# Performance work log

Hardware: AMD Instinct MI355X
Metric: run time of the kernel (lower is better)

The kernel has to match this reference:

```python
import jax, jax.numpy as jnp
import numpy as np


def _perceive(x):
    """Depthwise 3x3 perception: per channel emit (identity, dx, dy), matching
    tf.nn.depthwise_conv2d with kernel repeated along the in-channel axis, so
    output channel ordering is [c0_I, c0_dx, c0_dy, c1_I, ...]."""
    C = x.shape[-1]
    _i = jnp.array([0.0, 1.0, 0.0], dtype=x.dtype)
    I = jnp.outer(_i, _i)
    dx = jnp.outer(jnp.array([1.0, 2.0, 1.0], dtype=x.dtype),
                   jnp.array([-1.0, 0.0, 1.0], dtype=x.dtype)) / 8.0
    dy = dx.T
    base = jnp.stack([I, dx, dy], axis=-1)[:, :, None, :]  # [3,3,1,3]
    kernel = jnp.tile(base, (1, 1, 1, C))                   # [3,3,1,3C]
    # grouped conv with feature_group_count=C == depthwise conv, multiplier 3
    y = jax.lax.conv_general_dilated(
        x, kernel, window_strides=(1, 1), padding='SAME',
        dimension_numbers=('NHWC', 'HWIO', 'NHWC'), feature_group_count=C)
    return y  # [B,H,W,3C]


def setup_inputs() -> dict:
    key = jax.random.key(0)
    ks = jax.random.split(key, 6)
    B, H, W, C = 16, 256, 256, 16
    x = jax.random.normal(ks[0], (B, H, W, C), dtype=jnp.float32)
    # update mask: tf.random.normal(...) <= fire_rate (0.5), per pixel
    update_mask = jax.random.normal(ks[1], (B, H, W, 1), dtype=jnp.float32) <= 0.5
    # 1x1 conv weights (glorot-ish scale). NOTE: the original zero-initializes
    # w3/b3; we use small random values so the op is numerically non-trivial.
    w1 = jax.random.normal(ks[2], (3 * C, 4 * C), dtype=jnp.float32) / np.sqrt(3 * C)
    b1 = jnp.zeros((4 * C,), dtype=jnp.float32)
    w2 = jax.random.normal(ks[3], (4 * C, 2 * C), dtype=jnp.float32) / np.sqrt(4 * C)
    b2 = jnp.zeros((2 * C,), dtype=jnp.float32)
    w3 = jax.random.normal(ks[4], (2 * C, C), dtype=jnp.float32) / np.sqrt(2 * C)
    b3 = jnp.zeros((C,), dtype=jnp.float32)
    return {"x": x, "w1": w1, "b1": b1, "w2": w2, "b2": b2,
            "w3": w3, "b3": b3, "update_mask": update_mask}


def reference(x, w1, b1, w2, b2, w3, b3, update_mask):
    step_size = 1.0
    y = _perceive(x)  # [B,H,W,3C]
    h = jnp.tanh(jnp.einsum('bhwc,cd->bhwd', y, w1) + b1)
    h = jnp.tanh(jnp.einsum('bhwc,cd->bhwd', h, w2) + b2)
    dx = (jnp.einsum('bhwc,cd->bhwd', h, w3) + b3) * step_size
    return x + dx * update_mask.astype(x.dtype)
```

## Files before the change

### kernel.cpp

```cpp
#include <hip/hip_runtime.h>
#include <hip/hip_bf16.h>

typedef unsigned int u32;
typedef unsigned short u16;
typedef unsigned char u8;

typedef float f32x16 __attribute__((ext_vector_type(16)));
typedef short bf16x8 __attribute__((ext_vector_type(8)));

#define OFF_A1  0
#define OFF_A1B 18432
#define OFF_WT2 20480
#define OFF_WT3 25600
#define OFF_B3  27648
#define PREP_N  13840

__global__ void probe_kernel(const u16* __restrict__ w1h,
                             const u32* __restrict__ maskw,
                             u32* __restrict__ flags) {
  __shared__ int sg, su8, sbf;
  if (threadIdx.x == 0) { sg = 0; su8 = 0; sbf = 0; }
  __syncthreads();
  int g = 0;
#pragma unroll
  for (int i = 0; i < 8; ++i) {
    u16 h = w1h[threadIdx.x * 8 + i];
    int e = (h >> 7) & 0xFF;
    if (e >= 0xC0) g++;
  }
  if (g) atomicAdd(&sg, g);
  u32 w = maskw[threadIdx.x];
  bool bytes01 = ((w & 0xFEFEFEFEu) == 0u);
  int bsum = (int)(w & 1u) + (int)((w >> 8) & 1u) +
             (int)((w >> 16) & 1u) + (int)((w >> 24) & 1u);
  if (bytes01 && bsum >= 2) atomicAdd(&su8, 1);
  if (w == 0x3F803F80u || w == 0x00003F80u) atomicAdd(&sbf, 1);
  __syncthreads();
  if (threadIdx.x == 0) {
    flags[0] = (sg == 0) ? 1u : 0u;
    flags[1] = (su8 > 0) ? 1u : ((sbf > 0) ? 2u : 4u);
  }
}

__device__ __forceinline__ float bf2f(u16 h) {
  return __uint_as_float(((u32)h) << 16);
}
__device__ __forceinline__ u16 f2bf(float f) {
  u32 u = __float_as_uint(f);
  return (u16)((u + 0x7FFFu + ((u >> 16) & 1u)) >> 16);
}
__device__ __forceinline__ u32 pkbf(float a, float b) {
  u32 ua = __float_as_uint(a) + 0x8000u;
  u32 ub = __float_as_uint(b) + 0x8000u;
  return __builtin_amdgcn_perm(ub, ua, 0x07060302);
}
__device__ __forceinline__ float rdv(const void* s, int i, bool bf) {
  return bf ? bf2f(((const u16*)s)[i]) : ((const float*)s)[i];
}

__global__ void prep_weights(const void* __restrict__ w1, const void* __restrict__ b1,
                             const void* __restrict__ w2, const void* __restrict__ b2,
                             const void* __restrict__ w3, const void* __restrict__ b3,
                             const u32* __restrict__ flags, u8* __restrict__ Wb) {
  int i = blockIdx.x * 256 + threadIdx.x;
  if (i >= PREP_N) return;
  const bool bf = flags[0] != 0;
  if (i < 9216) {
    int off = i >> 10, rem = i & 1023;
    int mt = rem >> 9, hi = (rem >> 8) & 1, l = (rem >> 3) & 31, k8 = i & 7;
    int ch = mt * 32 + l, k = hi * 8 + k8;
    int oi = off / 3, oj = off % 3;
    const float axv[3] = {1.f, 2.f, 1.f};
    const float bxv[3] = {-1.f, 0.f, 1.f};
    float ci  = (oi == 1 && oj == 1) ? 1.f : 0.f;
    float dxv = axv[oi] * bxv[oj] * 0.125f;
    float dyv = axv[oj] * bxv[oi] * 0.125f;
    float v = ci  * rdv(w1, (3 * k + 0) * 64 + ch, bf)
            + dxv * rdv(w1, (3 * k + 1) * 64 + ch, bf)
            + dyv * rdv(w1, (3 * k + 2) * 64 + ch, bf);
    ((u16*)(Wb + OFF_A1))[i] = f2bf(v);
  } else if (i < 10240) {
    int j = i - 9216;
    int mt = j >> 9, l = (j >> 3) & 31;
    ((u16*)(Wb + OFF_A1B))[j] = f2bf(rdv(b1, mt * 32 + l, bf) * 0.0625f);
  } else if (i < 12800) {
    int j = i - 10240, n = j / 80, k = j - n * 80;
    float v;
    if (k < 64) {
      int s = k >> 4, hh = (k >> 3) & 1, q = (k & 7) >> 1, e = k & 1;
      int c = 32 * (s >> 1) + 8 * (2 * (s & 1) + (q >> 1)) + 4 * hh + 2 * (q & 1) + e;
      v = rdv(w2, c * 32 + n, bf);
    } else {
      v = (k == 64) ? rdv(b2, n, bf) : 0.0f;
    }
    ((u16*)(Wb + OFF_WT2))[j] = f2bf(v);
  } else if (i < 13824) {
    int j = i - 12800, n = j >> 5, k = j & 31;
    float v = 0.0f;
    if (n < 16) {
      int cout = (n & 3) + 4 * ((n >> 3) & 1) + 8 * ((n >> 2) & 1);
      int s = k >> 4, hh = (k >> 3) & 1, q = (k & 7) >> 1, e = k & 1;
      int cin = 8 * (2 * s + (q >> 1)) + 4 * hh + 2 * (q & 1) + e;
      v = rdv(w3, cin * 16 + cout, bf);
    }
    ((u16*)(Wb + OFF_WT3))[j] = f2bf(v);
  } else {
    int j = i - 13824;
    ((float*)(Wb + OFF_B3))[j] = rdv(b3, j, bf);
  }
}

__device__ __forceinline__ float fast_tanh(float x) {
  float e = __expf(2.0f * x);
  float r = __builtin_amdgcn_rcpf(e + 1.0f);
  return fmaf(-2.0f, r, 1.0f);
}

union U4 { uint4 q; u32 u[4]; bf16x8 h; float4 f; };

__device__ __forceinline__ void wave_lds_fence() {
  __builtin_amdgcn_wave_barrier();
  __asm__ __volatile__("s_waitcnt lgkmcnt(0)" ::: "memory");
  __builtin_amdgcn_wave_barrier();
}

#define MFMA(a, b, c) __builtin_amdgcn_mfma_f32_32x32x16_bf16((a), (b), (c), 0, 0, 0)

#define XS_STRIDE 8256
#define SCR_OFF   33024
#define SCR_WAVE  5120
#define LDS_TOTAL 53504

template <bool BF16>
__device__ __forceinline__ void nca_body(const void* __restrict__ xv,
                                         const u8* __restrict__ Wb,
                                         const void* __restrict__ maskv, int mw,
                                         void* __restrict__ outv,
                                         u8* __restrict__ xs) {
  const int tid = threadIdx.x;
  const int l   = tid & 63;
  const int wid = tid >> 6;
  const int l31 = l & 31;
  const int hi  = l >> 5;
  const int img   = blockIdx.x >> 7;
  const int r0    = (blockIdx.x & 127) << 1;

  if (tid < 8) {
    int rr = tid >> 1, side = tid & 1;
    uint4 z = make_uint4(0, 0, 0, 0);
    uint4* d = (uint4*)(xs + rr * XS_STRIDE + (side ? 257 : 0) * 32);
    d[0] = z; d[1] = z;
  }
#pragma unroll
  for (int rr = 0; rr < 4; ++rr) {
    int hr = r0 - 1 + rr;
    bool valid = (hr >= 0) && (hr <= 255);
    if (BF16) {
      const u16* src = (const u16*)xv + ((size_t)(img * 256 + hr) << 12);
#pragma unroll
      for (int s = 0; s < 2; ++s) {
        int c = s * 256 + tid;
        uint4 v = make_uint4(0, 0, 0, 0);
        if (valid) v = *(const uint4*)(src + c * 8);
        *(uint4*)(xs + rr * XS_STRIDE + ((c >> 1) + 1) * 32 + (c & 1) * 16) = v;
      }
    } else {
      const float* src = (const float*)xv + ((size_t)(img * 256 + hr) << 12);
#pragma unroll
      for (int k = 0; k < 4; ++k) {
        int q = k * 256 + tid;
        uint2 w = make_uint2(0, 0);
        if (valid) {
          float4 v = *(const float4*)(src + q * 4);
          w.x = pkbf(v.x, v.y); w.y = pkbf(v.z, v.w);
        }
        *(uint2*)(xs + rr * XS_STRIDE + ((q >> 2) + 1) * 32 + (q & 3) * 8) = w;
      }
    }
  }
  __syncthreads();

  const int sr      = wid >> 1;
  const int colbase = (wid & 1) * 128;
  const int gr      = img * 256 + r0 + sr;
  const int growpix = gr << 8;

  bf16x8 A1b[2];
#pragma unroll
  for (int mt = 0; mt < 2; ++mt) {
    U4 t; t.q = *(const uint4*)(Wb + OFF_A1B + ((mt * 2 + hi) * 32 + l31) * 16);
    A1b[mt] = t.h;
  }
  U4 ones; ones.u[0] = ones.u[1] = ones.u[2] = ones.u[3] = 0x3F803F80u;
  const float* B3f = (const float*)(Wb + OFF_B3);
  float4 b3lo = *(const float4*)(B3f + 8 * hi);
  float4 b3hi4 = *(const float4*)(B3f + 8 * hi + 4);
  u8* scr = xs + SCR_OFF + wid * SCR_WAVE;

#pragma unroll
  for (int tp = 0; tp < 2; ++tp) {
#pragma unroll
    for (int u = 0; u < 2; ++u) {
      const int cb = colbase + (tp * 2 + u) * 32;

      f32x16 c0 = {0,0,0,0,0,0,0,0,0,0,0,0,0,0,0,0};
      f32x16 c1 = {0,0,0,0,0,0,0,0,0,0,0,0,0,0,0,0};
      c0 = MFMA(A1b[0], ones.h, c0);
      c1 = MFMA(A1b[1], ones.h, c1);
#pragma unroll
      for (int off = 0; off < 9; ++off) {
        const int oi = off / 3, oj = off % 3;
        U4 bx; bx.q = *(const uint4*)(xs + (sr + oi) * XS_STRIDE +
                                      (cb + l31 + oj) * 32 + hi * 16);
        U4 a0; a0.q = *(const uint4*)(Wb + OFF_A1 + (((off * 2 + 0) * 2 + hi) * 32 + l31) * 16);
        U4 a1; a1.q = *(const uint4*)(Wb + OFF_A1 + (((off * 2 + 1) * 2 + hi) * 32 + l31) * 16);
        c0 = MFMA(a0.h, bx.h, c0);
        c1 = MFMA(a1.h, bx.h, c1);
      }

      u32 o1[16];
#pragma unroll
      for (int g = 0; g < 4; ++g)
#pragma unroll
        for (int pp = 0; pp < 2; ++pp) {
          o1[g * 2 + pp]     = pkbf(fast_tanh(c0[g * 4 + 2 * pp]), fast_tanh(c0[g * 4 + 2 * pp + 1]));
          o1[8 + g * 2 + pp] = pkbf(fast_tanh(c1[g * 4 + 2 * pp]), fast_tanh(c1[g * 4 + 2 * pp + 1]));
        }

      f32x16 c2 = {0,0,0,0,0,0,0,0,0,0,0,0,0,0,0,0};
#pragma unroll
      for (int s = 0; s < 4; ++s) {
        U4 a2; a2.q = *(const uint4*)(Wb + OFF_WT2 + l31 * 160 + s * 32 + hi * 16);
        U4 bfr; bfr.u[0] = o1[4*s]; bfr.u[1] = o1[4*s+1]; bfr.u[2] = o1[4*s+2]; bfr.u[3] = o1[4*s+3];
        c2 = MFMA(a2.h, bfr.h, c2);
      }
      {
        U4 a2; a2.q = *(const uint4*)(Wb + OFF_WT2 + l31 * 160 + 4 * 32 + hi * 16);
        U4 bb; bb.u[0] = hi ? 0u : 0x00003F80u; bb.u[1] = 0; bb.u[2] = 0; bb.u[3] = 0;
        c2 = MFMA(a2.h, bb.h, c2);
      }
      u32 o2[8];
#pragma unroll
      for (int g = 0; g < 4; ++g)
#pragma unroll
        for (int pp = 0; pp < 2; ++pp)
          o2[g * 2 + pp] = pkbf(fast_tanh(c2[g * 4 + 2 * pp]), fast_tanh(c2[g * 4 + 2 * pp + 1]));

      f32x16 c3 = {0,0,0,0,0,0,0,0,0,0,0,0,0,0,0,0};
#pragma unroll
      for (int s = 0; s < 2; ++s) {
        U4 a3; a3.q = *(const uint4*)(Wb + OFF_WT3 + l31 * 64 + s * 32 + hi * 16);
        U4 bfr; bfr.u[0] = o2[4*s]; bfr.u[1] = o2[4*s+1]; bfr.u[2] = o2[4*s+2]; bfr.u[3] = o2[4*s+3];
        c3 = MFMA(a3.h, bfr.h, c3);
      }

      U4 w0, w1;
      w0.f.x = c3[0] + b3lo.x;  w0.f.y = c3[1] + b3lo.y;
      w0.f.z = c3[2] + b3lo.z;  w0.f.w = c3[3] + b3lo.w;
      w1.f.x = c3[4] + b3hi4.x; w1.f.y = c3[5] + b3hi4.y;
      w1.f.z = c3[6] + b3hi4.z; w1.f.w = c3[7] + b3hi4.w;
      u8* sa = scr + (u * 32 + l31) * 80 + hi * 32;
      *(float4*)(sa) = w0.f;
      *(float4*)(sa + 16) = w1.f;
    }
    wave_lds_fence();

    const int cb2 = colbase + tp * 64;
#pragma unroll
    for (int P = 0; P < 4; ++P) {
      const int px_l = P * 16 + (l >> 2);
      const int qd   = l & 3;
      float4 dx = *(const float4*)(scr + px_l * 80 + qd * 16);
      const int gpx = growpix + cb2 + px_l;
      bool ms;
      if (mw == 1)      ms = ((const u8*)maskv)[gpx] != 0;
      else if (mw == 2) ms = ((const u16*)maskv)[gpx] != 0;
      else              ms = ((const u32*)maskv)[gpx] != 0;
      const float mf = ms ? 1.0f : 0.0f;
      const int e = gpx * 16 + qd * 4;
      if (BF16) {
        uint2 xu = *(const uint2*)((const u16*)xv + e);
        float x0 = bf2f((u16)(xu.x & 0xFFFF)), x1 = bf2f((u16)(xu.x >> 16));
        float x2 = bf2f((u16)(xu.y & 0xFFFF)), x3 = bf2f((u16)(xu.y >> 16));
        float o0 = fmaf(dx.x, mf, x0), o1v = fmaf(dx.y, mf, x1);
        float o2v = fmaf(dx.z, mf, x2), o3v = fmaf(dx.w, mf, x3);
        uint2 w; w.x = pkbf(o0, o1v); w.y = pkbf(o2v, o3v);
        *(uint2*)((u16*)outv + e) = w;
      } else {
        float4 xc = *(const float4*)((const float*)xv + e);
        float4 o;
        o.x = fmaf(dx.x, mf, xc.x); o.y = fmaf(dx.y, mf, xc.y);
        o.z = fmaf(dx.z, mf, xc.z); o.w = fmaf(dx.w, mf, xc.w);
        *(float4*)((float*)outv + e) = o;
      }
    }
    wave_lds_fence();
  }
}

__global__ __launch_bounds__(256, 3) void nca_main(const void* __restrict__ xv,
                                                   const u8* __restrict__ Wb,
                                                   const void* __restrict__ maskv,
                                                   const u32* __restrict__ flags,
                                                   void* __restrict__ outv) {
  __shared__ __align__(16) u8 smem[LDS_TOTAL];
  const bool isbf = flags[0] != 0;
  const int mw = (int)flags[1];
  if (isbf) nca_body<true>(xv, Wb, maskv, mw, outv, smem);
  else      nca_body<false>(xv, Wb, maskv, mw, outv, smem);
}

extern "C" void kernel_launch(void* const* d_in, const int* in_sizes, int n_in,
                              void* d_out, int out_size, void* d_ws, size_t ws_size,
                              hipStream_t stream) {
  u32* flags = (u32*)d_ws;
  u8* Wb = (u8*)d_ws + 64;

  probe_kernel<<<1, 256, 0, stream>>>((const u16*)d_in[1], (const u32*)d_in[7], flags);

  prep_weights<<<(PREP_N + 255) / 256, 256, 0, stream>>>(
      d_in[1], d_in[2], d_in[3], d_in[4], d_in[5], d_in[6], flags, Wb);

  const int pixels = in_sizes[7];
  const int blocks = pixels / 512;
  nca_main<<<blocks, 256, 0, stream>>>(d_in[0], Wb, d_in[7], flags, d_out);
}
```

Measured before the change: 216.6 us.

## Fold probe into kernels, write outputs from MFMA registers, drop LDS scratch

```diff
diff --git a/kernel.cpp b/kernel.cpp
--- a/kernel.cpp
+++ b/kernel.cpp
@@ -15,33 +15,6 @@
 #define OFF_B3  27648
 #define PREP_N  13840
 
-__global__ void probe_kernel(const u16* __restrict__ w1h,
-                             const u32* __restrict__ maskw,
-                             u32* __restrict__ flags) {
-  __shared__ int sg, su8, sbf;
-  if (threadIdx.x == 0) { sg = 0; su8 = 0; sbf = 0; }
-  __syncthreads();
-  int g = 0;
-#pragma unroll
-  for (int i = 0; i < 8; ++i) {
-    u16 h = w1h[threadIdx.x * 8 + i];
-    int e = (h >> 7) & 0xFF;
-    if (e >= 0xC0) g++;
-  }
-  if (g) atomicAdd(&sg, g);
-  u32 w = maskw[threadIdx.x];
-  bool bytes01 = ((w & 0xFEFEFEFEu) == 0u);
-  int bsum = (int)(w & 1u) + (int)((w >> 8) & 1u) +
-             (int)((w >> 16) & 1u) + (int)((w >> 24) & 1u);
-  if (bytes01 && bsum >= 2) atomicAdd(&su8, 1);
-  if (w == 0x3F803F80u || w == 0x00003F80u) atomicAdd(&sbf, 1);
-  __syncthreads();
-  if (threadIdx.x == 0) {
-    flags[0] = (sg == 0) ? 1u : 0u;
-    flags[1] = (su8 > 0) ? 1u : ((sbf > 0) ? 2u : 4u);
-  }
-}
-
 __device__ __forceinline__ float bf2f(u16 h) {
   return __uint_as_float(((u32)h) << 16);
 }
@@ -61,10 +34,26 @@
 __global__ void prep_weights(const void* __restrict__ w1, const void* __restrict__ b1,
                              const void* __restrict__ w2, const void* __restrict__ b2,
                              const void* __restrict__ w3, const void* __restrict__ b3,
-                             const u32* __restrict__ flags, u8* __restrict__ Wb) {
+                             u8* __restrict__ Wb) {
+  __shared__ int sg;
+  if (threadIdx.x == 0) sg = 0;
+  __syncthreads();
+  {
+    const u16* w1h = (const u16*)w1;
+    int g = 0;
+#pragma unroll
+    for (int k = 0; k < 8; ++k) {
+      u16 h = w1h[threadIdx.x * 8 + k];
+      int e = (h >> 7) & 0xFF;
+      if (e >= 0xC0) g++;
+    }
+    if (g) atomicAdd(&sg, g);
+  }
+  __syncthreads();
+  const bool bf = (sg == 0);
+
   int i = blockIdx.x * 256 + threadIdx.x;
   if (i >= PREP_N) return;
-  const bool bf = flags[0] != 0;
   if (i < 9216) {
     int off = i >> 10, rem = i & 1023;
     int mt = rem >> 9, hi = (rem >> 8) & 1, l = (rem >> 3) & 31, k8 = i & 7;
@@ -118,32 +107,24 @@
 
 union U4 { uint4 q; u32 u[4]; bf16x8 h; float4 f; };
 
-__device__ __forceinline__ void wave_lds_fence() {
-  __builtin_amdgcn_wave_barrier();
-  __asm__ __volatile__("s_waitcnt lgkmcnt(0)" ::: "memory");
-  __builtin_amdgcn_wave_barrier();
-}
-
 #define MFMA(a, b, c) __builtin_amdgcn_mfma_f32_32x32x16_bf16((a), (b), (c), 0, 0, 0)
 
 #define XS_STRIDE 8256
-#define SCR_OFF   33024
-#define SCR_WAVE  5120
-#define LDS_TOTAL 53504
+#define LDS_TOTAL 33024
 
 template <bool BF16>
 __device__ __forceinline__ void nca_body(const void* __restrict__ xv,
                                          const u8* __restrict__ Wb,
                                          const void* __restrict__ maskv, int mw,
                                          void* __restrict__ outv,
-                                         u8* __restrict__ xs) {
+                                         u8* __restrict__ xs, int wg) {
   const int tid = threadIdx.x;
   const int l   = tid & 63;
   const int wid = tid >> 6;
   const int l31 = l & 31;
   const int hi  = l >> 5;
-  const int img   = blockIdx.x >> 7;
-  const int r0    = (blockIdx.x & 127) << 1;
+  const int img   = wg >> 7;
+  const int r0    = (wg & 127) << 1;
 
   if (tid < 8) {
     int rr = tid >> 1, side = tid & 1;
@@ -193,15 +174,36 @@
   }
   U4 ones; ones.u[0] = ones.u[1] = ones.u[2] = ones.u[3] = 0x3F803F80u;
   const float* B3f = (const float*)(Wb + OFF_B3);
-  float4 b3lo = *(const float4*)(B3f + 8 * hi);
+  float4 b3lo  = *(const float4*)(B3f + 8 * hi);
   float4 b3hi4 = *(const float4*)(B3f + 8 * hi + 4);
-  u8* scr = xs + SCR_OFF + wid * SCR_WAVE;
 
 #pragma unroll
   for (int tp = 0; tp < 2; ++tp) {
 #pragma unroll
     for (int u = 0; u < 2; ++u) {
       const int cb = colbase + (tp * 2 + u) * 32;
+      const int gpx = growpix + cb + l31;
+      const int e = gpx * 16 + hi * 8;
+
+      bool ms;
+      if (mw == 1)      ms = ((const u8*)maskv)[gpx] != 0;
+      else if (mw == 2) ms = ((const u16*)maskv)[gpx] != 0;
+      else              ms = ((const u32*)maskv)[gpx] != 0;
+      const float mf = ms ? 1.0f : 0.0f;
+      float xr0, xr1, xr2, xr3, xr4, xr5, xr6, xr7;
+      if (BF16) {
+        uint4 xu = *(const uint4*)((const u16*)xv + e);
+        xr0 = bf2f((u16)(xu.x & 0xFFFF)); xr1 = bf2f((u16)(xu.x >> 16));
+        xr2 = bf2f((u16)(xu.y & 0xFFFF)); xr3 = bf2f((u16)(xu.y >> 16));
+        xr4 = bf2f((u16)(xu.z & 0xFFFF)); xr5 = bf2f((u16)(xu.z >> 16));
+        xr6 = bf2f((u16)(xu.w & 0xFFFF)); xr7 = bf2f((u16)(xu.w >> 16));
+      } else {
+        const float* xp = (const float*)xv + e;
+        float4 xa = *(const float4*)(xp);
+        float4 xb = *(const float4*)(xp + 4);
+        xr0 = xa.x; xr1 = xa.y; xr2 = xa.z; xr3 = xa.w;
+        xr4 = xb.x; xr5 = xb.y; xr6 = xb.z; xr7 = xb.w;
+      }
 
       f32x16 c0 = {0,0,0,0,0,0,0,0,0,0,0,0,0,0,0,0};
       f32x16 c1 = {0,0,0,0,0,0,0,0,0,0,0,0,0,0,0,0};
@@ -254,74 +256,81 @@
         c3 = MFMA(a3.h, bfr.h, c3);
       }
 
-      U4 w0, w1;
-      w0.f.x = c3[0] + b3lo.x;  w0.f.y = c3[1] + b3lo.y;
-      w0.f.z = c3[2] + b3lo.z;  w0.f.w = c3[3] + b3lo.w;
-      w1.f.x = c3[4] + b3hi4.x; w1.f.y = c3[5] + b3hi4.y;
-      w1.f.z = c3[6] + b3hi4.z; w1.f.w = c3[7] + b3hi4.w;
-      u8* sa = scr + (u * 32 + l31) * 80 + hi * 32;
-      *(float4*)(sa) = w0.f;
-      *(float4*)(sa + 16) = w1.f;
-    }
-    wave_lds_fence();
-
-    const int cb2 = colbase + tp * 64;
-#pragma unroll
-    for (int P = 0; P < 4; ++P) {
-      const int px_l = P * 16 + (l >> 2);
-      const int qd   = l & 3;
-      float4 dx = *(const float4*)(scr + px_l * 80 + qd * 16);
-      const int gpx = growpix + cb2 + px_l;
-      bool ms;
-      if (mw == 1)      ms = ((const u8*)maskv)[gpx] != 0;
-      else if (mw == 2) ms = ((const u16*)maskv)[gpx] != 0;
-      else              ms = ((const u32*)maskv)[gpx] != 0;
-      const float mf = ms ? 1.0f : 0.0f;
-      const int e = gpx * 16 + qd * 4;
+      float d0 = c3[0] + b3lo.x,  d1 = c3[1] + b3lo.y;
+      float d2 = c3[2] + b3lo.z,  d3 = c3[3] + b3lo.w;
+      float d4 = c3[4] + b3hi4.x, d5 = c3[5] + b3hi4.y;
+      float d6 = c3[6] + b3hi4.z, d7 = c3[7] + b3hi4.w;
       if (BF16) {
-        uint2 xu = *(const uint2*)((const u16*)xv + e);
-        float x0 = bf2f((u16)(xu.x & 0xFFFF)), x1 = bf2f((u16)(xu.x >> 16));
-        float x2 = bf2f((u16)(xu.y & 0xFFFF)), x3 = bf2f((u16)(xu.y >> 16));
-        float o0 = fmaf(dx.x, mf, x0), o1v = fmaf(dx.y, mf, x1);
-        float o2v = fmaf(dx.z, mf, x2), o3v = fmaf(dx.w, mf, x3);
-        uint2 w; w.x = pkbf(o0, o1v); w.y = pkbf(o2v, o3v);
-        *(uint2*)((u16*)outv + e) = w;
+        uint4 w;
+        w.x = pkbf(fmaf(d0, mf, xr0), fmaf(d1, mf, xr1));
+        w.y = pkbf(fmaf(d2, mf, xr2), fmaf(d3, mf, xr3));
+        w.z = pkbf(fmaf(d4, mf, xr4), fmaf(d5, mf, xr5));
+        w.w = pkbf(fmaf(d6, mf, xr6), fmaf(d7, mf, xr7));
+        *(uint4*)((u16*)outv + e) = w;
       } else {
-        float4 xc = *(const float4*)((const float*)xv + e);
-        float4 o;
-        o.x = fmaf(dx.x, mf, xc.x); o.y = fmaf(dx.y, mf, xc.y);
-        o.z = fmaf(dx.z, mf, xc.z); o.w = fmaf(dx.w, mf, xc.w);
-        *(float4*)((float*)outv + e) = o;
-      }
-    }
-    wave_lds_fence();
-  }
-}
-
-__global__ __launch_bounds__(256, 3) void nca_main(const void* __restrict__ xv,
+        float4 oa, ob;
+        oa.x = fmaf(d0, mf, xr0); oa.y = fmaf(d1, mf, xr1);
+        oa.z = fmaf(d2, mf, xr2); oa.w = fmaf(d3, mf, xr3);
+        ob.x = fmaf(d4, mf, xr4); ob.y = fmaf(d5, mf, xr5);
+        ob.z = fmaf(d6, mf, xr6); ob.w = fmaf(d7, mf, xr7);
+        float* op = (float*)outv + e;
+        *(float4*)(op) = oa;
+        *(float4*)(op + 4) = ob;
+      }
+    }
+  }
+}
+
+__global__ __launch_bounds__(256, 4) void nca_main(const void* __restrict__ xv,
+                                                   const u16* __restrict__ w1h,
                                                    const u8* __restrict__ Wb,
                                                    const void* __restrict__ maskv,
-                                                   const u32* __restrict__ flags,
                                                    void* __restrict__ outv) {
   __shared__ __align__(16) u8 smem[LDS_TOTAL];
-  const bool isbf = flags[0] != 0;
-  const int mw = (int)flags[1];
-  if (isbf) nca_body<true>(xv, Wb, maskv, mw, outv, smem);
-  else      nca_body<false>(xv, Wb, maskv, mw, outv, smem);
+  __shared__ int sg, su8, sbf;
+  if (threadIdx.x == 0) { sg = 0; su8 = 0; sbf = 0; }
+  __syncthreads();
+  {
+    int g = 0;
+#pragma unroll
+    for (int k = 0; k < 8; ++k) {
+      u16 h = w1h[threadIdx.x * 8 + k];
+      int e = (h >> 7) & 0xFF;
+      if (e >= 0xC0) g++;
+    }
+    if (g) atomicAdd(&sg, g);
+    u32 w = ((const u32*)maskv)[threadIdx.x];
+    bool bytes01 = ((w & 0xFEFEFEFEu) == 0u);
+    int bsum = (int)(w & 1u) + (int)((w >> 8) & 1u) +
+               (int)((w >> 16) & 1u) + (int)((w >> 24) & 1u);
+    if (bytes01 && bsum >= 2) atomicAdd(&su8, 1);
+    if (w == 0x3F803F80u || w == 0x00003F80u) atomicAdd(&sbf, 1);
+  }
+  __syncthreads();
+  const bool isbf = (sg == 0);
+  const int mw = (su8 > 0) ? 1 : ((sbf > 0) ? 2 : 4);
+
+  int wg = blockIdx.x;
+  const int nwg = gridDim.x;
+  if ((nwg & 7) == 0) {
+    const int cpx = nwg >> 3;
+    wg = (wg & 7) * cpx + (wg >> 3);
+  }
+
+  if (isbf) nca_body<true>(xv, Wb, maskv, mw, outv, smem, wg);
+  else      nca_body<false>(xv, Wb, maskv, mw, outv, smem, wg);
 }
 
 extern "C" void kernel_launch(void* const* d_in, const int* in_sizes, int n_in,
                               void* d_out, int out_size, void* d_ws, size_t ws_size,
                               hipStream_t stream) {
-  u32* flags = (u32*)d_ws;
   u8* Wb = (u8*)d_ws + 64;
 
-  probe_kernel<<<1, 256, 0, stream>>>((const u16*)d_in[1], (const u32*)d_in[7], flags);
-
   prep_weights<<<(PREP_N + 255) / 256, 256, 0, stream>>>(
-      d_in[1], d_in[2], d_in[3], d_in[4], d_in[5], d_in[6], flags, Wb);
+      d_in[1], d_in[2], d_in[3], d_in[4], d_in[5], d_in[6], Wb);
 
   const int pixels = in_sizes[7];
   const int blocks = pixels / 512;
-  nca_main<<<blocks, 256, 0, stream>>>(d_in[0], Wb, d_in[7], flags, d_out);
-}
+  nca_main<<<blocks, 256, 0, stream>>>(d_in[0], (const u16*)d_in[1], Wb,
+                                       d_in[7], d_out);
+}
```

Result: slower. 235.5 us (+8.7%).
